# Kernel tuning notes

Measured on AMD Instinct MI355X. Metric: run time of the kernel, lower is better.

## Reference

```python
import jax, jax.numpy as jnp
import numpy as np

SEQ, BATCH, V = 200, 4096, 50000


def setup_inputs() -> dict:
    key = jax.random.key(0)
    k_text, k_w, k_b = jax.random.split(key, 3)
    text = jax.random.randint(k_text, (SEQ, BATCH), 0, V, dtype=jnp.int64 if jax.config.jax_enable_x64 else jnp.int32)
    w_weight = jax.random.normal(k_w, (1, V), dtype=jnp.float32) * 0.05
    w_bias = jax.random.normal(k_b, (1,), dtype=jnp.float32) * 0.05
    return {"text": text, "w_weight": w_weight, "w_bias": w_bias}


def reference(text, w_weight, w_bias):
    # text: [seq, batch] int token ids; w_weight: [1, V]; w_bias: [1]
    seq, batch = text.shape
    vocab = w_weight.shape[1]
    # Counter over unique tokens per document with +=1 per unique value
    # => binary PRESENCE matrix [batch, V] (duplicates collapse to 1).
    presence = jnp.zeros((batch, vocab), dtype=jnp.float32)
    presence = presence.at[jnp.arange(batch)[None, :], text].set(1.0)
    # Linear(V, 1): [batch, V] @ [V, 1] + bias -> [batch, 1]
    return presence @ w_weight.T + w_bias
```

## Files before the change

### kernel.cpp

```cpp
#include <hip/hip_runtime.h>


#define SEQ 200
#define BATCH 4096
#define TABLE 512

__global__ __launch_bounds__(256) void MNB_24111946400019_kernel(
    const int* __restrict__ text,
    const float* __restrict__ w,
    const float* __restrict__ bias,
    float* __restrict__ out)
{
    __shared__ int table[TABLE];
    __shared__ float partial[4];

    const int b = blockIdx.x;
    const int t = threadIdx.x;

    table[t] = -1;
    table[t + 256] = -1;
    __syncthreads();

    float sum = 0.0f;
    if (t < SEQ) {
        const int tok = text[t * BATCH + b];
        unsigned h = ((unsigned)tok * 2654435761u) >> 23;
        for (;;) {
            int prev = atomicCAS(&table[h], -1, tok);
            if (prev == -1) { sum = w[tok]; break; }
            if (prev == tok) break;
            h = (h + 1) & (TABLE - 1);
        }
    }

    #pragma unroll
    for (int off = 32; off > 0; off >>= 1)
        sum += __shfl_down(sum, off, 64);

    const int wave = t >> 6;
    const int lane = t & 63;
    if (lane == 0) partial[wave] = sum;
    __syncthreads();

    if (t == 0) {
        out[b] = partial[0] + partial[1] + partial[2] + partial[3] + bias[0];
    }
}

extern "C" void kernel_launch(void* const* d_in, const int* in_sizes, int n_in,
                              void* d_out, int out_size, void* d_ws, size_t ws_size,
                              hipStream_t stream) {
    const int*   text = (const int*)d_in[0];
    const float* w    = (const float*)d_in[1];
    const float* bias = (const float*)d_in[2];
    float* out = (float*)d_out;

    MNB_24111946400019_kernel<<<BATCH, 256, 0, stream>>>(text, w, bias, out);
}
```

Measured before the change: 66.31 us.

## Process eight batch columns per block with staged coalesced loads and table scan

Each block now handles eight documents instead of one. It loads the token ids as 32-byte contiguous rows per sequence position, which replaces 4-byte strided reads, and keeps eight per-column hash tables in LDS. Dedup inserts no longer fetch weights. Instead a second pass scans each 512-slot table with 32 lanes and sums w for the occupied slots, then does a half-wave shuffle reduction. This cuts the grid to 512 blocks and raises LDS use per block, which may reduce occupancy and parallelism.

Result: no change. 65.44 us (-1.3%).

```diff
diff --git a/kernel.cpp b/kernel.cpp
--- a/kernel.cpp
+++ b/kernel.cpp
@@ -1,9 +1,11 @@
 #include <hip/hip_runtime.h>
 
 
-#define SEQ 200
-#define BATCH 4096
-#define TABLE 512
+#define SEQ    200
+#define BATCH  4096
+#define COLS   8
+#define TSLOTS 512
+#define NTOK   (SEQ * COLS)
 
 __global__ __launch_bounds__(256) void MNB_24111946400019_kernel(
     const int* __restrict__ text,
@@ -11,40 +13,53 @@
     const float* __restrict__ bias,
     float* __restrict__ out)
 {
-    __shared__ int table[TABLE];
-    __shared__ float partial[4];
+    __shared__ int staged[NTOK];
+    __shared__ int table[COLS * TSLOTS];
 
-    const int b = blockIdx.x;
-    const int t = threadIdx.x;
+    const int t  = threadIdx.x;
+    const int c0 = blockIdx.x * COLS;
 
-    table[t] = -1;
-    table[t + 256] = -1;
+    {
+        const int4 m1 = make_int4(-1, -1, -1, -1);
+        int4* tb = (int4*)table;
+        #pragma unroll
+        for (int i = 0; i < 4; ++i) tb[t + 256 * i] = m1;
+    }
+
+    for (int idx = t; idx < NTOK; idx += 256) {
+        const int s = idx >> 3;
+        const int j = idx & (COLS - 1);
+        staged[idx] = text[s * BATCH + c0 + j];
+    }
     __syncthreads();
 
+    for (int idx = t; idx < NTOK; idx += 256) {
+        const int tok = staged[idx];
+        const int j   = idx & (COLS - 1);
+        unsigned h = ((unsigned)tok * 2654435761u) >> 23;
+        int* tb = &table[j * TSLOTS];
+        for (;;) {
+            const int prev = atomicCAS(&tb[h], -1, tok);
+            if (prev == -1 || prev == tok) break;
+            h = (h + 1) & (TSLOTS - 1);
+        }
+    }
+    __syncthreads();
+
+    const int j = t >> 5;
+    const int l = t & 31;
     float sum = 0.0f;
-    if (t < SEQ) {
-        const int tok = text[t * BATCH + b];
-        unsigned h = ((unsigned)tok * 2654435761u) >> 23;
-        for (;;) {
-            int prev = atomicCAS(&table[h], -1, tok);
-            if (prev == -1) { sum = w[tok]; break; }
-            if (prev == tok) break;
-            h = (h + 1) & (TABLE - 1);
-        }
+    #pragma unroll
+    for (int k = 0; k < TSLOTS / 32; ++k) {
+        const int tok = table[j * TSLOTS + l + 32 * k];
+        if (tok >= 0) sum += w[tok];
     }
 
     #pragma unroll
-    for (int off = 32; off > 0; off >>= 1)
-        sum += __shfl_down(sum, off, 64);
+    for (int off = 16; off > 0; off >>= 1)
+        sum += __shfl_xor(sum, off, 64);
 
-    const int wave = t >> 6;
-    const int lane = t & 63;
-    if (lane == 0) partial[wave] = sum;
-    __syncthreads();
-
-    if (t == 0) {
-        out[b] = partial[0] + partial[1] + partial[2] + partial[3] + bias[0];
-    }
+    if (l == 0) out[c0 + j] = sum + bias[0];
 }
 
 extern "C" void kernel_launch(void* const* d_in, const int* in_sizes, int n_in,
@@ -55,5 +70,5 @@
     const float* bias = (const float*)d_in[2];
     float* out = (float*)d_out;
 
-    MNB_24111946400019_kernel<<<BATCH, 256, 0, stream>>>(text, w, bias, out);
+    MNB_24111946400019_kernel<<<BATCH / COLS, 256, 0, stream>>>(text, w, bias, out);
 }
```
